# Optimization experiments

Hardware: AMD Instinct MI355X
Metric: run time of the kernel (lower is better)

The kernel has to match this reference:

```python
import jax, jax.numpy as jnp
import numpy as np

B, S, H = 4, 2048, 2048
FFN, E, TOP_K = 5632, 8, 2

def setup_inputs() -> dict:
    key = jax.random.key(0)
    k1, k2, k3, k4, k5 = jax.random.split(key, 5)
    return {
        "hidden_states": jax.random.normal(k1, (B, S, H), dtype=jnp.float32),
        "wg": jax.random.normal(k2, (H, E), dtype=jnp.float32) * 0.02,
        "wg_ema": jnp.zeros((H, E), dtype=jnp.float32),
        "fc1_1": jax.random.normal(k3, (E, FFN, H), dtype=jnp.float32) * 0.02,
        "fc1_2": jax.random.normal(k4, (E, FFN, H), dtype=jnp.float32) * 0.02,
        "fc2": jax.random.normal(k5, (E, H, FFN), dtype=jnp.float32) * 0.02,
    }

def reference(hidden_states, wg, wg_ema, fc1_1, fc1_2, fc2):
    b, s, h = hidden_states.shape
    x = hidden_states.reshape(-1, h)  # [T, H]
    # Router: P6TopkCapGate mixes the live gate with its EMA 50/50.
    wg_running = 0.5 * (wg_ema + wg.astype(jnp.float32))
    router_logits = x.astype(jnp.float32) @ wg_running  # [T, E]
    probs = jax.nn.softmax(router_logits, axis=-1)
    top_vals, top_idx = jax.lax.top_k(probs, TOP_K)  # [T, K]
    routing_weights = (top_vals / top_vals.sum(axis=-1, keepdims=True)).astype(x.dtype)
    out = jnp.zeros_like(x)
    n_experts = fc1_1.shape[0]
    for e in range(n_experts):
        # combine weight per token for this expert (0 if not routed here)
        w_e = jnp.sum(routing_weights * (top_idx == e), axis=-1)  # [T]
        h1 = x @ fc1_1[e].T            # [T, FFN]
        h2 = x @ fc1_2[e].T            # [T, FFN]
        y = (jax.nn.silu(h1) * h2) @ fc2[e].T  # [T, H]
        out = out + w_e[:, None] * y
    return out.reshape(b, s, h), router_logits
```

## Files before the change

### kernel.cpp

```cpp
#include <hip/hip_runtime.h>
#include <stdint.h>

#define TT 8192
#define HD 2048
#define FFN 5632
#define NE 8
#define NPK 11264

typedef float f32x4 __attribute__((ext_vector_type(4)));
typedef _Float16 f16x8 __attribute__((ext_vector_type(8)));
typedef unsigned int u32;

#define OFF_WR    0ul
#define OFF_CNT   65536ul
#define OFF_LISTS 66048ul
#define OFF_TOKW  328192ul
#define OFF_ACT   1048576ul
#define OFF_XH    (OFF_ACT + 184549376ul)
#define OFF_WPK   (OFF_XH + 33554432ul)
#define OFF_W3H   OFF_WPK

__device__ __forceinline__ void gl_lds16(const void* g, void* s) {
  __builtin_amdgcn_global_load_lds((const __attribute__((address_space(1))) u32*)g,
                                   (__attribute__((address_space(3))) u32*)s, 16, 0, 0);
}

__device__ __forceinline__ f16x8 cvt8(f32x4 a, f32x4 b) {
  f16x8 r;
  r[0] = (_Float16)a[0]; r[1] = (_Float16)a[1]; r[2] = (_Float16)a[2]; r[3] = (_Float16)a[3];
  r[4] = (_Float16)b[0]; r[5] = (_Float16)b[1]; r[6] = (_Float16)b[2]; r[7] = (_Float16)b[3];
  return r;
}

__global__ __launch_bounds__(256) void k_cvt(const float* __restrict__ in,
                                             _Float16* __restrict__ out, long n8) {
  long i = (long)blockIdx.x * 256 + threadIdx.x;
  const long stride = (long)gridDim.x * 256;
  for (; i < n8; i += stride) {
    f32x4 a = ((const f32x4*)in)[i * 2];
    f32x4 b = ((const f32x4*)in)[i * 2 + 1];
    ((f16x8*)out)[i] = cvt8(a, b);
  }
}

__global__ __launch_bounds__(256) void k_cvtpack(const float* __restrict__ fc11,
                                                 const float* __restrict__ fc12,
                                                 _Float16* __restrict__ wpk) {
  const long total = (long)NE * NPK * 256;
  long i8 = (long)blockIdx.x * 256 + threadIdx.x;
  const long stride = (long)gridDim.x * 256;
  for (; i8 < total; i8 += stride) {
    int k8 = (int)(i8 & 255);
    long qe = i8 >> 8;
    int q = (int)(qe % NPK);
    int e = (int)(qe / NPK);
    int c = q & 127;
    int f = (q >> 7) * 64 + ((c >> 6) & 1) * 32 + ((c >> 4) & 1) * 16 + (c & 15);
    const float* src = ((c >> 5) & 1 ? fc12 : fc11) + ((size_t)e * FFN + f) * HD + k8 * 8;
    f32x4 a = *(const f32x4*)src;
    f32x4 b = *(const f32x4*)(src + 4);
    *(f16x8*)(wpk + qe * HD + (size_t)k8 * 8) = cvt8(a, b);
  }
}

__global__ __launch_bounds__(256) void k_prep(const float* __restrict__ wg,
                                              const float* __restrict__ wge,
                                              float* __restrict__ wr) {
  int i = blockIdx.x * 256 + threadIdx.x;
  if (i < HD * NE) wr[i] = 0.5f * (wge[i] + wg[i]);
}

__global__ __launch_bounds__(256) void k_router(const float* __restrict__ x,
                                                const float* __restrict__ wr,
                                                float* __restrict__ logits,
                                                float* __restrict__ tokw,
                                                int* __restrict__ lists,
                                                int* __restrict__ cnt,
                                                _Float16* __restrict__ xh) {
  const int t = blockIdx.x, tid = threadIdx.x;
  const float* xr = x + (size_t)t * HD;
  _Float16* xo = xh + (size_t)t * HD;
  float acc[NE];
#pragma unroll
  for (int e = 0; e < NE; ++e) acc[e] = 0.f;
  for (int h = tid; h < HD; h += 256) {
    float xv = xr[h];
    xo[h] = (_Float16)xv;
    const float* w = wr + h * NE;
#pragma unroll
    for (int e = 0; e < NE; ++e) acc[e] = fmaf(xv, w[e], acc[e]);
  }
#pragma unroll
  for (int e = 0; e < NE; ++e)
#pragma unroll
    for (int off = 32; off; off >>= 1)
      acc[e] += __shfl_xor(acc[e], off, 64);
  __shared__ float red[4][NE];
  int wv = tid >> 6;
  if ((tid & 63) == 0)
    for (int e = 0; e < NE; ++e) red[wv][e] = acc[e];
  __syncthreads();
  if (tid == 0) {
    float l[NE];
#pragma unroll
    for (int e = 0; e < NE; ++e) l[e] = red[0][e] + red[1][e] + red[2][e] + red[3][e];
#pragma unroll
    for (int e = 0; e < NE; ++e) logits[(size_t)t * NE + e] = l[e];
    int i0 = 0;
    for (int e = 1; e < NE; ++e) if (l[e] > l[i0]) i0 = e;
    int i1 = -1;
    for (int e = 0; e < NE; ++e) if (e != i0 && (i1 < 0 || l[e] > l[i1])) i1 = e;
    float p1 = __expf(l[i1] - l[i0]);
    float s = 1.f + p1;
    tokw[t * 2]     = 1.f / s;
    tokw[t * 2 + 1] = p1 / s;
    int q0 = atomicAdd(&cnt[i0], 1);
    lists[i0 * TT + q0] = t * 2;
    int q1 = atomicAdd(&cnt[i1], 1);
    lists[i1 * TT + q1] = t * 2 + 1;
  }
}

__global__ __launch_bounds__(256, 3) void k_ffn1(const _Float16* __restrict__ xh,
                                                 const _Float16* __restrict__ wpk,
                                                 const int* __restrict__ lists,
                                                 const int* __restrict__ cnt,
                                                 _Float16* __restrict__ act) {
  const int bid = blockIdx.x;
  const int xk = bid & 7;
  const int sq = bid >> 3;
  const int slot = sq / 264;
  const int within = sq - slot * 264;
  const int ct = within / 3;
  const int rt_in = within - ct * 3;
  const int e = slot & 7;
  const int r = ((xk - e) & 7) + ((slot >> 3) << 3);
  const int rt = r * 3 + rt_in;
  const int count = cnt[e];
  if (rt * 192 >= count) return;
  const int tid = threadIdx.x, lane = tid & 63, wv = tid >> 6;

  __shared__ __align__(16) _Float16 As[2][6144];
  __shared__ __align__(16) _Float16 Bs[2][4096];
  __shared__ int row_pair[192];

  if (tid < 192) {
    int rg = rt * 192 + tid;
    row_pair[tid] = (rg < count) ? lists[e * TT + rg] : -1;
  }
  __syncthreads();

  const int lr = lane >> 2;
  const int cpA = (lane & 3) ^ (((wv * 48 + lr) >> 1) & 3);
  const int srowA = wv * 48 + lr;
  const int pA0 = row_pair[srowA], pA1 = row_pair[srowA + 16], pA2 = row_pair[srowA + 32];
  const _Float16* gA0 = xh + (size_t)(pA0 >= 0 ? (pA0 >> 1) : 0) * HD + cpA * 8;
  const _Float16* gA1 = xh + (size_t)(pA1 >= 0 ? (pA1 >> 1) : 0) * HD + cpA * 8;
  const _Float16* gA2 = xh + (size_t)(pA2 >= 0 ? (pA2 >> 1) : 0) * HD + cpA * 8;
  const int srowB = wv * 32 + lr;
  const int cpB = (lane & 3) ^ ((srowB >> 1) & 3);
  const _Float16* gB0 = wpk + ((size_t)e * NPK + (size_t)ct * 128 + srowB) * HD + cpB * 8;
  const _Float16* gB1 = gB0 + (size_t)16 * HD;

  auto stage = [&](int sl, int k0) {
    gl_lds16(gA0 + k0, &As[sl][wv * 1536]);
    gl_lds16(gA1 + k0, &As[sl][wv * 1536 + 512]);
    gl_lds16(gA2 + k0, &As[sl][wv * 1536 + 1024]);
    gl_lds16(gB0 + k0, &Bs[sl][wv * 1024]);
    gl_lds16(gB1 + k0, &Bs[sl][wv * 1024 + 512]);
  };

  const f32x4 z4 = {0.f, 0.f, 0.f, 0.f};
  f32x4 acc[6][4];
#pragma unroll
  for (int m = 0; m < 6; ++m)
#pragma unroll
    for (int n = 0; n < 4; ++n) acc[m][n] = z4;

  const int fr = lane & 15, kq = lane >> 4;
  const int wrow = (wv >> 1) * 96, wcol = (wv & 1) * 64;
  int aoff[6], boff[4];
#pragma unroll
  for (int m = 0; m < 6; ++m) {
    int rr = wrow + m * 16 + fr;
    aoff[m] = rr * 32 + (kq ^ ((rr >> 1) & 3)) * 8;
  }
#pragma unroll
  for (int n = 0; n < 4; ++n) {
    int rr = wcol + n * 16 + fr;
    boff[n] = rr * 32 + (kq ^ ((rr >> 1) & 3)) * 8;
  }

  stage(0, 0);
  __syncthreads();

  const int NS = HD / 32;
  for (int ks = 0; ks < NS; ++ks) {
    const int buf = ks & 1;
    if (ks + 1 < NS) stage(buf ^ 1, (ks + 1) * 32);
    f16x8 fa[6], fb[4];
#pragma unroll
    for (int m = 0; m < 6; ++m) fa[m] = *(const f16x8*)&As[buf][aoff[m]];
#pragma unroll
    for (int n = 0; n < 4; ++n) fb[n] = *(const f16x8*)&Bs[buf][boff[n]];
    __builtin_amdgcn_s_setprio(1);
#pragma unroll
    for (int m = 0; m < 6; ++m)
#pragma unroll
      for (int n = 0; n < 4; ++n)
        acc[m][n] = __builtin_amdgcn_mfma_f32_16x16x32_f16(fa[m], fb[n], acc[m][n], 0, 0, 0);
    __builtin_amdgcn_s_setprio(0);
    __syncthreads();
  }

  const int wn = wv & 1;
  const int rbase = wrow + kq * 4;
#pragma unroll
  for (int m = 0; m < 6; ++m) {
#pragma unroll
    for (int n = 0; n < 2; ++n) {
      const int f = ct * 64 + wn * 32 + n * 16 + fr;
#pragma unroll
      for (int j = 0; j < 4; ++j) {
        int rl = rbase + m * 16 + j;
        int pr = row_pair[rl];
        if (pr >= 0) {
          float h1 = acc[m][n][j], h2 = acc[m][n + 2][j];
          float sv = h1 / (1.f + __expf(-h1));
          act[(size_t)pr * FFN + f] = (_Float16)(sv * h2);
        }
      }
    }
  }
}

__global__ __launch_bounds__(256, 3) void k_ffn2(const _Float16* __restrict__ act,
                                                 const _Float16* __restrict__ w3h,
                                                 const int* __restrict__ lists,
                                                 const int* __restrict__ cnt,
                                                 const float* __restrict__ tokw,
                                                 float* __restrict__ out) {
  const int bid = blockIdx.x;
  const int xk = bid & 7;
  const int sq = bid >> 3;
  const int e = sq / 88;
  const int within = sq - e * 88;
  const int rt = within >> 1;
  const int ct = (((xk - e) & 7) << 1) + (within & 1);
  const int count = cnt[e];
  if (rt * 192 >= count) return;
  const int tid = threadIdx.x, lane = tid & 63, wv = tid >> 6;

  __shared__ __align__(16) _Float16 As[2][6144];
  __shared__ __align__(16) _Float16 Bs[2][4096];
  __shared__ int row_pair[192];
  __shared__ float row_w[192];

  if (tid < 192) {
    int rg = rt * 192 + tid;
    int pr = (rg < count) ? lists[e * TT + rg] : -1;
    row_pair[tid] = pr;
    row_w[tid] = (pr >= 0) ? tokw[pr] : 0.f;
  }
  __syncthreads();

  const int lr = lane >> 2;
  const int srowA = wv * 48 + lr;
  const int cpA = (lane & 3) ^ ((srowA >> 1) & 3);
  const int pA0 = row_pair[srowA], pA1 = row_pair[srowA + 16], pA2 = row_pair[srowA + 32];
  const _Float16* gA0 = act + (size_t)(pA0 >= 0 ? pA0 : 0) * FFN + cpA * 8;
  const _Float16* gA1 = act + (size_t)(pA1 >= 0 ? pA1 : 0) * FFN + cpA * 8;
  const _Float16* gA2 = act + (size_t)(pA2 >= 0 ? pA2 : 0) * FFN + cpA * 8;
  const int srowB = wv * 32 + lr;
  const int cpB = (lane & 3) ^ ((srowB >> 1) & 3);
  const _Float16* gB0 = w3h + ((size_t)e * HD + (size_t)ct * 128 + srowB) * FFN + cpB * 8;
  const _Float16* gB1 = gB0 + (size_t)16 * FFN;

  auto stage = [&](int sl, int k0) {
    gl_lds16(gA0 + k0, &As[sl][wv * 1536]);
    gl_lds16(gA1 + k0, &As[sl][wv * 1536 + 512]);
    gl_lds16(gA2 + k0, &As[sl][wv * 1536 + 1024]);
    gl_lds16(gB0 + k0, &Bs[sl][wv * 1024]);
    gl_lds16(gB1 + k0, &Bs[sl][wv * 1024 + 512]);
  };

  const f32x4 z4 = {0.f, 0.f, 0.f, 0.f};
  f32x4 acc[6][4];
#pragma unroll
  for (int m = 0; m < 6; ++m)
#pragma unroll
    for (int n = 0; n < 4; ++n) acc[m][n] = z4;

  const int fr = lane & 15, kq = lane >> 4;
  const int wrow = (wv >> 1) * 96, wcol = (wv & 1) * 64;
  int aoff[6], boff[4];
#pragma unroll
  for (int m = 0; m < 6; ++m) {
    int rr = wrow + m * 16 + fr;
    aoff[m] = rr * 32 + (kq ^ ((rr >> 1) & 3)) * 8;
  }
#pragma unroll
  for (int n = 0; n < 4; ++n) {
    int rr = wcol + n * 16 + fr;
    boff[n] = rr * 32 + (kq ^ ((rr >> 1) & 3)) * 8;
  }

  stage(0, 0);
  __syncthreads();

  const int NS = FFN / 32;
  for (int ks = 0; ks < NS; ++ks) {
    const int buf = ks & 1;
    if (ks + 1 < NS) stage(buf ^ 1, (ks + 1) * 32);
    f16x8 fa[6], fb[4];
#pragma unroll
    for (int m = 0; m < 6; ++m) fa[m] = *(const f16x8*)&As[buf][aoff[m]];
#pragma unroll
    for (int n = 0; n < 4; ++n) fb[n] = *(const f16x8*)&Bs[buf][boff[n]];
    __builtin_amdgcn_s_setprio(1);
#pragma unroll
    for (int m = 0; m < 6; ++m)
#pragma unroll
      for (int n = 0; n < 4; ++n)
        acc[m][n] = __builtin_amdgcn_mfma_f32_16x16x32_f16(fa[m], fb[n], acc[m][n], 0, 0, 0);
    __builtin_amdgcn_s_setprio(0);
    __syncthreads();
  }

  const int rbase = wrow + kq * 4;
#pragma unroll
  for (int m = 0; m < 6; ++m) {
#pragma unroll
    for (int n = 0; n < 4; ++n) {
      const int col = ct * 128 + wcol + n * 16 + fr;
#pragma unroll
      for (int j = 0; j < 4; ++j) {
        int rl = rbase + m * 16 + j;
        int pr = row_pair[rl];
        if (pr >= 0) {
          float v = acc[m][n][j] * row_w[rl];
          unsafeAtomicAdd(out + (size_t)(pr >> 1) * HD + col, v);
        }
      }
    }
  }
}

extern "C" void kernel_launch(void* const* d_in, const int* in_sizes, int n_in,
                              void* d_out, int out_size, void* d_ws, size_t ws_size,
                              hipStream_t stream) {
  (void)in_sizes; (void)n_in; (void)out_size; (void)ws_size;
  const float* x    = (const float*)d_in[0];
  const float* wg   = (const float*)d_in[1];
  const float* wge  = (const float*)d_in[2];
  const float* fc11 = (const float*)d_in[3];
  const float* fc12 = (const float*)d_in[4];
  const float* fc2  = (const float*)d_in[5];
  float* out    = (float*)d_out;
  float* logits = out + (size_t)TT * HD;

  char* ws = (char*)d_ws;
  float* wr      = (float*)(ws + OFF_WR);
  int*   cnt     = (int*)(ws + OFF_CNT);
  int*   lists   = (int*)(ws + OFF_LISTS);
  float* tokw    = (float*)(ws + OFF_TOKW);
  _Float16* act  = (_Float16*)(ws + OFF_ACT);
  _Float16* xh   = (_Float16*)(ws + OFF_XH);
  _Float16* wpk  = (_Float16*)(ws + OFF_WPK);
  _Float16* w3h  = (_Float16*)(ws + OFF_W3H);

  hipMemsetAsync(out, 0, (size_t)TT * HD * sizeof(float), stream);
  hipMemsetAsync(cnt, 0, NE * sizeof(int), stream);

  k_prep<<<dim3((HD * NE + 255) / 256), 256, 0, stream>>>(wg, wge, wr);
  k_router<<<dim3(TT), 256, 0, stream>>>(x, wr, logits, tokw, lists, cnt, xh);

  k_cvtpack<<<dim3(2048), 256, 0, stream>>>(fc11, fc12, wpk);

  k_ffn1<<<dim3(8 * 16 * 264), 256, 0, stream>>>(xh, wpk, lists, cnt, act);

  k_cvt<<<dim3(2048), 256, 0, stream>>>(fc2, w3h, (long)NE * HD * FFN / 8);

  k_ffn2<<<dim3(8 * 8 * 88), 256, 0, stream>>>(act, w3h, lists, cnt, tokw, out);
}
```

Baseline: 1.931 ms.

## Enlarge ffn1 tile to 256x256 with 512 threads and triple-buffered LDS pipeline

Rewrites the gate/up GEMM kernel to use 512-thread blocks computing 256-row by 256-column (128 FFN pairs) tiles instead of 192x128. The weight packing changes to match, and the K loop moves to a three-stage LDS ring with split A/B staging, explicit vmcnt waits and raw barriers between half-tile MFMA phases. The aim is higher arithmetic intensity per loaded byte and better overlap of global loads with MFMA work. In exchange it uses more LDS per block, fewer blocks, and more padding waste on partial row tiles for small expert counts.

```diff
diff --git a/kernel.cpp b/kernel.cpp
--- a/kernel.cpp
+++ b/kernel.cpp
@@ -24,6 +24,9 @@
   __builtin_amdgcn_global_load_lds((const __attribute__((address_space(1))) u32*)g,
                                    (__attribute__((address_space(3))) u32*)s, 16, 0, 0);
 }
+
+#define VM4() asm volatile("s_waitcnt vmcnt(4)" ::: "memory")
+#define VM0() asm volatile("s_waitcnt vmcnt(0)" ::: "memory")
 
 __device__ __forceinline__ f16x8 cvt8(f32x4 a, f32x4 b) {
   f16x8 r;
@@ -54,8 +57,8 @@
     long qe = i8 >> 8;
     int q = (int)(qe % NPK);
     int e = (int)(qe / NPK);
-    int c = q & 127;
-    int f = (q >> 7) * 64 + ((c >> 6) & 1) * 32 + ((c >> 4) & 1) * 16 + (c & 15);
+    int c = q & 255;
+    int f = (q >> 8) * 128 + ((c >> 6) & 3) * 32 + ((c >> 4) & 1) * 16 + (c & 15);
     const float* src = ((c >> 5) & 1 ? fc12 : fc11) + ((size_t)e * FFN + f) * HD + k8 * 8;
     f32x4 a = *(const f32x4*)src;
     f32x4 b = *(const f32x4*)(src + 4);
@@ -121,7 +124,7 @@
   }
 }
 
-__global__ __launch_bounds__(256, 3) void k_ffn1(const _Float16* __restrict__ xh,
+__global__ __launch_bounds__(512, 2) void k_ffn1(const _Float16* __restrict__ xh,
                                                  const _Float16* __restrict__ wpk,
                                                  const int* __restrict__ lists,
                                                  const int* __restrict__ cnt,
@@ -129,97 +132,113 @@
   const int bid = blockIdx.x;
   const int xk = bid & 7;
   const int sq = bid >> 3;
-  const int slot = sq / 264;
-  const int within = sq - slot * 264;
-  const int ct = within / 3;
-  const int rt_in = within - ct * 3;
+  const int slot = sq / 88;
+  const int within = sq - slot * 88;
+  const int ct = within >> 1;
+  const int rt_in = within & 1;
   const int e = slot & 7;
   const int r = ((xk - e) & 7) + ((slot >> 3) << 3);
-  const int rt = r * 3 + rt_in;
+  const int rt = r * 2 + rt_in;
   const int count = cnt[e];
-  if (rt * 192 >= count) return;
+  if (rt * 256 >= count) return;
   const int tid = threadIdx.x, lane = tid & 63, wv = tid >> 6;
 
-  __shared__ __align__(16) _Float16 As[2][6144];
-  __shared__ __align__(16) _Float16 Bs[2][4096];
-  __shared__ int row_pair[192];
-
-  if (tid < 192) {
-    int rg = rt * 192 + tid;
+  __shared__ __align__(16) _Float16 As[3][8192];
+  __shared__ __align__(16) _Float16 Bs[3][8192];
+  __shared__ int row_pair[256];
+
+  if (tid < 256) {
+    int rg = rt * 256 + tid;
     row_pair[tid] = (rg < count) ? lists[e * TT + rg] : -1;
   }
   __syncthreads();
 
   const int lr = lane >> 2;
-  const int cpA = (lane & 3) ^ (((wv * 48 + lr) >> 1) & 3);
-  const int srowA = wv * 48 + lr;
-  const int pA0 = row_pair[srowA], pA1 = row_pair[srowA + 16], pA2 = row_pair[srowA + 32];
-  const _Float16* gA0 = xh + (size_t)(pA0 >= 0 ? (pA0 >> 1) : 0) * HD + cpA * 8;
-  const _Float16* gA1 = xh + (size_t)(pA1 >= 0 ? (pA1 >> 1) : 0) * HD + cpA * 8;
-  const _Float16* gA2 = xh + (size_t)(pA2 >= 0 ? (pA2 >> 1) : 0) * HD + cpA * 8;
-  const int srowB = wv * 32 + lr;
-  const int cpB = (lane & 3) ^ ((srowB >> 1) & 3);
-  const _Float16* gB0 = wpk + ((size_t)e * NPK + (size_t)ct * 128 + srowB) * HD + cpB * 8;
-  const _Float16* gB1 = gB0 + (size_t)16 * HD;
-
-  auto stage = [&](int sl, int k0) {
-    gl_lds16(gA0 + k0, &As[sl][wv * 1536]);
-    gl_lds16(gA1 + k0, &As[sl][wv * 1536 + 512]);
-    gl_lds16(gA2 + k0, &As[sl][wv * 1536 + 1024]);
-    gl_lds16(gB0 + k0, &Bs[sl][wv * 1024]);
-    gl_lds16(gB1 + k0, &Bs[sl][wv * 1024 + 512]);
+  const int r0 = wv * 16 + lr;
+  const int cp = (((lane & 3) ^ ((r0 >> 1) & 3))) * 8;
+  const int pr0 = row_pair[r0], pr1 = row_pair[r0 + 128];
+  const _Float16* gA0 = xh + (size_t)(pr0 >= 0 ? (pr0 >> 1) : 0) * HD + cp;
+  const _Float16* gA1 = xh + (size_t)(pr1 >= 0 ? (pr1 >> 1) : 0) * HD + cp;
+  const _Float16* gB0 = wpk + ((size_t)e * NPK + (size_t)ct * 256 + r0) * HD + cp;
+  const _Float16* gB1 = gB0 + (size_t)128 * HD;
+
+  auto stgA = [&](int b, int k0) {
+    gl_lds16(gA0 + k0, &As[b][wv * 512]);
+    gl_lds16(gA1 + k0, &As[b][4096 + wv * 512]);
   };
+  auto stgB = [&](int b, int k0) {
+    gl_lds16(gB0 + k0, &Bs[b][wv * 512]);
+    gl_lds16(gB1 + k0, &Bs[b][4096 + wv * 512]);
+  };
 
   const f32x4 z4 = {0.f, 0.f, 0.f, 0.f};
-  f32x4 acc[6][4];
-#pragma unroll
-  for (int m = 0; m < 6; ++m)
+  f32x4 acc[8][4];
+#pragma unroll
+  for (int m = 0; m < 8; ++m)
 #pragma unroll
     for (int n = 0; n < 4; ++n) acc[m][n] = z4;
 
   const int fr = lane & 15, kq = lane >> 4;
-  const int wrow = (wv >> 1) * 96, wcol = (wv & 1) * 64;
-  int aoff[6], boff[4];
-#pragma unroll
-  for (int m = 0; m < 6; ++m) {
-    int rr = wrow + m * 16 + fr;
-    aoff[m] = rr * 32 + (kq ^ ((rr >> 1) & 3)) * 8;
+  const int wm = wv >> 2, wn = wv & 3;
+  int aoff[8], boff[4];
+#pragma unroll
+  for (int m = 0; m < 8; ++m) {
+    int R = wm * 128 + m * 16 + fr;
+    aoff[m] = R * 32 + (kq ^ ((R >> 1) & 3)) * 8;
   }
 #pragma unroll
   for (int n = 0; n < 4; ++n) {
-    int rr = wcol + n * 16 + fr;
-    boff[n] = rr * 32 + (kq ^ ((rr >> 1) & 3)) * 8;
-  }
-
-  stage(0, 0);
-  __syncthreads();
+    int R = wn * 64 + n * 16 + fr;
+    boff[n] = R * 32 + (kq ^ ((R >> 1) & 3)) * 8;
+  }
+
+  stgA(0, 0); stgB(0, 0);
+  stgA(1, 32); stgB(1, 32);
+  VM4();
+  __builtin_amdgcn_s_barrier();
 
   const int NS = HD / 32;
-  for (int ks = 0; ks < NS; ++ks) {
-    const int buf = ks & 1;
-    if (ks + 1 < NS) stage(buf ^ 1, (ks + 1) * 32);
-    f16x8 fa[6], fb[4];
-#pragma unroll
-    for (int m = 0; m < 6; ++m) fa[m] = *(const f16x8*)&As[buf][aoff[m]];
-#pragma unroll
-    for (int n = 0; n < 4; ++n) fb[n] = *(const f16x8*)&Bs[buf][boff[n]];
+  for (int s = 0; s < NS; ++s) {
+    const int b = s % 3;
+    const int pb = (s + 2) % 3;
+    const bool pre = (s + 2 < NS);
+    f16x8 fa0[4], fb[4];
+#pragma unroll
+    for (int m = 0; m < 4; ++m) fa0[m] = *(const f16x8*)&As[b][aoff[m]];
+#pragma unroll
+    for (int n = 0; n < 4; ++n) fb[n] = *(const f16x8*)&Bs[b][boff[n]];
+    if (pre) stgA(pb, (s + 2) * 32);
+    __builtin_amdgcn_s_barrier();
     __builtin_amdgcn_s_setprio(1);
 #pragma unroll
-    for (int m = 0; m < 6; ++m)
+    for (int m = 0; m < 4; ++m)
 #pragma unroll
       for (int n = 0; n < 4; ++n)
-        acc[m][n] = __builtin_amdgcn_mfma_f32_16x16x32_f16(fa[m], fb[n], acc[m][n], 0, 0, 0);
+        acc[m][n] = __builtin_amdgcn_mfma_f32_16x16x32_f16(fa0[m], fb[n], acc[m][n], 0, 0, 0);
     __builtin_amdgcn_s_setprio(0);
-    __syncthreads();
-  }
-
-  const int wn = wv & 1;
-  const int rbase = wrow + kq * 4;
-#pragma unroll
-  for (int m = 0; m < 6; ++m) {
+    __builtin_amdgcn_s_barrier();
+    f16x8 fa1[4];
+#pragma unroll
+    for (int m = 0; m < 4; ++m) fa1[m] = *(const f16x8*)&As[b][aoff[m + 4]];
+    if (pre) { stgB(pb, (s + 2) * 32); VM4(); }
+    else if (s == NS - 2) { VM0(); }
+    __builtin_amdgcn_s_barrier();
+    __builtin_amdgcn_s_setprio(1);
+#pragma unroll
+    for (int m = 0; m < 4; ++m)
+#pragma unroll
+      for (int n = 0; n < 4; ++n)
+        acc[m + 4][n] = __builtin_amdgcn_mfma_f32_16x16x32_f16(fa1[m], fb[n], acc[m + 4][n], 0, 0, 0);
+    __builtin_amdgcn_s_setprio(0);
+    __builtin_amdgcn_s_barrier();
+  }
+
+  const int rbase = wm * 128 + kq * 4;
+#pragma unroll
+  for (int m = 0; m < 8; ++m) {
 #pragma unroll
     for (int n = 0; n < 2; ++n) {
-      const int f = ct * 64 + wn * 32 + n * 16 + fr;
+      const int f = ct * 128 + wn * 32 + n * 16 + fr;
 #pragma unroll
       for (int j = 0; j < 4; ++j) {
         int rl = rbase + m * 16 + j;
@@ -377,7 +396,7 @@
 
   k_cvtpack<<<dim3(2048), 256, 0, stream>>>(fc11, fc12, wpk);
 
-  k_ffn1<<<dim3(8 * 16 * 264), 256, 0, stream>>>(xh, wpk, lists, cnt, act);
+  k_ffn1<<<dim3(8 * 16 * 88), 512, 0, stream>>>(xh, wpk, lists, cnt, act);
 
   k_cvt<<<dim3(2048), 256, 0, stream>>>(fc2, w3h, (long)NE * HD * FFN / 8);
 
```

New measurement: 2.025 ms. +4.9%, slower.
